# Kernel optimization log

Hardware: AMD Instinct MI355X
Metric: run time of the kernel (lower is better)

Reference implementation:

```python
import jax, jax.numpy as jnp
import numpy as np

NEG_SLOPE = 0.01  # F.leaky_relu default
DROP_P = 0.5      # F.dropout(p=0.5, training=True by default in this code)


def _lrelu(x):
    return jnp.where(x >= 0, x, NEG_SLOPE * x)


def _hconv(Xi, X, Ht, Hs, edge_w, theta, w_trans, bias):
    # Faithful to Ht.T @ diag(edge_w) @ Hs @ X @ theta + Xi @ w_trans + bias,
    # with diag(edge_w) fused as a per-row scale of the [E, out] intermediate.
    msg = (Hs @ X) @ theta                 # [E, out]
    agg = Ht.T @ (edge_w[:, None] * msg)   # [N, out]
    return _lrelu(agg + Xi @ w_trans + bias)


def setup_inputs() -> dict:
    key = jax.random.key(0)
    ks = jax.random.split(key, 14)
    N, E, F0, H = 8192, 4096, 128, 128
    f32 = jnp.float32
    return {
        "xi": jax.random.normal(ks[0], (N, F0), f32),
        "x": jax.random.normal(ks[1], (N, F0), f32),
        "Ht": jax.random.uniform(ks[2], (E, N), f32),
        "Hs": jax.random.uniform(ks[3], (E, N), f32),
        "state": jax.random.normal(ks[4], (N, 1), f32),
        # conv0 params (std=0.01 init as in torch code)
        "w_trans0": 0.01 * jax.random.normal(ks[5], (F0, H), f32),
        "theta0": 0.01 * jax.random.normal(ks[6], (F0, H), f32),
        "edge_w0": jnp.ones((E,), f32),
        "bias0": 0.01 * jax.random.normal(ks[7], (H,), f32),
        # conv1 params
        "w_trans1": 0.01 * jax.random.normal(ks[8], (H, H), f32),
        "theta1": 0.01 * jax.random.normal(ks[9], (H, H), f32),
        "edge_w1": jnp.ones((E,), f32),
        "bias1": 0.01 * jax.random.normal(ks[10], (H,), f32),
        # fc: Linear(H+1, 1)
        "fc_w": 0.01 * jax.random.normal(ks[11], (H + 1, 1), f32),
        "fc_b": 0.01 * jax.random.normal(ks[12], (1,), f32),
    }


def reference(xi, x, Ht, Hs, state,
              w_trans0, theta0, edge_w0, bias0,
              w_trans1, theta1, edge_w1, bias1,
              fc_w, fc_b):
    X1 = _hconv(xi, x, Ht, Hs, edge_w0, theta0, w_trans0, bias0)  # [N, H]
    # F.dropout(p=0.5) is active (training=True default); fixed mask for determinism
    keep = jax.random.bernoulli(jax.random.key(42), 1.0 - DROP_P, X1.shape)
    X1 = jnp.where(keep, X1 / (1.0 - DROP_P), 0.0)
    X2 = _hconv(xi, X1, Ht, Hs, edge_w1, theta1, w_trans1, bias1)  # [N, H]
    X = _lrelu(X2)  # second leaky_relu, as in DQN.forward
    Xc = jnp.concatenate([X, state], axis=1)  # [N, H+1]
    return Xc @ fc_w + fc_b  # [N, 1]
```

## Files before the change

### kernel.cpp

```cpp
#include <hip/hip_runtime.h>
#include <hip/hip_bf16.h>
#include <stdint.h>


typedef short short8 __attribute__((ext_vector_type(8)));
typedef float f32x4 __attribute__((ext_vector_type(4)));

static constexpr int N = 8192, E = 4096, F = 128;
static constexpr int SA = 8, SB = 4;

__device__ __forceinline__ unsigned rotl32(unsigned x, int r) {
  return (x << r) | (x >> (32 - r));
}

__device__ __forceinline__ uint2 threefry2x32(unsigned k0, unsigned k1,
                                              unsigned x0, unsigned x1) {
  unsigned ks[3] = {k0, k1, k0 ^ k1 ^ 0x1BD11BDAu};
  x0 += ks[0];
  x1 += ks[1];
  const int R0[4] = {13, 15, 26, 6};
  const int R1[4] = {17, 29, 16, 24};
#pragma unroll
  for (int i = 0; i < 5; ++i) {
#pragma unroll
    for (int j = 0; j < 4; ++j) {
      const int r = (i % 2 == 0) ? R0[j] : R1[j];
      x0 += x1;
      x1 = rotl32(x1, r);
      x1 ^= x0;
    }
    x0 += ks[(i + 1) % 3];
    x1 += ks[(i + 2) % 3] + (unsigned)(i + 1);
  }
  return make_uint2(x0, x1);
}

__device__ __forceinline__ float drop_scale(unsigned idx) {
  const uint2 o = threefry2x32(0u, 42u, 0u, idx);
  return ((o.x ^ o.y) & 0x80000000u) ? 0.0f : 2.0f;
}

__device__ __forceinline__ float lrelu(float v) {
  return v >= 0.0f ? v : 0.01f * v;
}

__device__ __forceinline__ unsigned rne1(float a) {
  unsigned ua = __builtin_bit_cast(unsigned, a);
  ua += 0x7fffu + ((ua >> 16) & 1u);
  return ua >> 16;
}
__device__ __forceinline__ float bf16_val(unsigned u16) {
  return __builtin_bit_cast(float, u16 << 16);
}
__device__ __forceinline__ unsigned pk_bf16(float a, float b) {
  return rne1(a) | (rne1(b) << 16);
}
__device__ __forceinline__ void split2(float a, float b, unsigned& hi,
                                       unsigned& lo) {
  const unsigned ha = rne1(a), hb = rne1(b);
  const float ra = a - bf16_val(ha), rb = b - bf16_val(hb);
  hi = ha | (hb << 16);
  lo = rne1(ra) | (rne1(rb) << 16);
}

template <bool TRANSA>
__global__ __launch_bounds__(256) void big_gemm(
    const float* __restrict__ A, const float* __restrict__ Bt,
    float* __restrict__ P, int M, int K, int lda, int kchunk) {
  __shared__ __align__(16) short As[128 * 40];
  __shared__ __align__(16) short Bh[128 * 40];
  __shared__ __align__(16) short Bl[128 * 40];

  const int tid = threadIdx.x;
  const int lane = tid & 63;
  const int w = tid >> 6;
  const int wm = (w & 1) << 6;
  const int wn = (w >> 1) << 6;
  const int l15 = lane & 15;
  const int koff = (lane >> 4) << 3;

  const int r0 = blockIdx.x * 128;
  const int s = blockIdx.y;
  const int kbeg = s * kchunk;
  const int kend = kbeg + kchunk;

  f32x4 acc[4][4];
#pragma unroll
  for (int i = 0; i < 4; ++i)
#pragma unroll
    for (int j = 0; j < 4; ++j) acc[i][j] = (f32x4){0.f, 0.f, 0.f, 0.f};

  for (int k0 = kbeg; k0 < kend; k0 += 32) {
    if (!TRANSA) {
#pragma unroll
      for (int i = 0; i < 4; ++i) {
        const int f = i * 256 + tid;
        const int m = f >> 3;
        const int kq = f & 7;
        const float4 v =
            *(const float4*)(A + (size_t)(r0 + m) * lda + k0 + 4 * kq);
        uint2 u = {pk_bf16(v.x, v.y), pk_bf16(v.z, v.w)};
        *(uint2*)&As[m * 40 + 4 * kq] = u;
      }
    } else {
#pragma unroll
      for (int i = 0; i < 2; ++i) {
        const int f = i * 256 + tid;
        const int m = f & 127;
        const int eo = f >> 7;
        float vv[8];
#pragma unroll
        for (int r = 0; r < 8; ++r)
          vv[r] = A[(size_t)(k0 + 8 * eo + r) * lda + (r0 + m)];
        uint4 u = {pk_bf16(vv[0], vv[1]), pk_bf16(vv[2], vv[3]),
                   pk_bf16(vv[4], vv[5]), pk_bf16(vv[6], vv[7])};
        *(uint4*)&As[m * 40 + 8 * eo] = u;
      }
    }
#pragma unroll
    for (int i = 0; i < 4; ++i) {
      const int q = i * 256 + tid;
      const int c = q >> 3;
      const int kq = q & 7;
      const float4 v = *(const float4*)(Bt + (size_t)c * K + k0 + 4 * kq);
      uint2 uh, ul;
      split2(v.x, v.y, uh.x, ul.x);
      split2(v.z, v.w, uh.y, ul.y);
      *(uint2*)&Bh[c * 40 + 4 * kq] = uh;
      *(uint2*)&Bl[c * 40 + 4 * kq] = ul;
    }
    __syncthreads();

    short8 af[4], bh[4], bl[4];
#pragma unroll
    for (int i = 0; i < 4; ++i)
      af[i] = *(const short8*)&As[(wm + 16 * i + l15) * 40 + koff];
#pragma unroll
    for (int j = 0; j < 4; ++j) {
      bh[j] = *(const short8*)&Bh[(wn + 16 * j + l15) * 40 + koff];
      bl[j] = *(const short8*)&Bl[(wn + 16 * j + l15) * 40 + koff];
    }
#pragma unroll
    for (int i = 0; i < 4; ++i)
#pragma unroll
      for (int j = 0; j < 4; ++j) {
        acc[i][j] = __builtin_amdgcn_mfma_f32_16x16x32_bf16(af[i], bl[j],
                                                            acc[i][j], 0, 0, 0);
        acc[i][j] = __builtin_amdgcn_mfma_f32_16x16x32_bf16(af[i], bh[j],
                                                            acc[i][j], 0, 0, 0);
      }
    __syncthreads();
  }

  const int rquad = (lane >> 4) << 2;
#pragma unroll
  for (int i = 0; i < 4; ++i)
#pragma unroll
    for (int j = 0; j < 4; ++j)
#pragma unroll
      for (int r = 0; r < 4; ++r) {
        const int row = r0 + wm + 16 * i + rquad + r;
        const int col = wn + 16 * j + l15;
        P[((size_t)s * M + row) * 128 + col] = acc[i][j][r];
      }
}

template <bool WA>
__global__ __launch_bounds__(256) void small_gemm(
    const float* __restrict__ src, const float* __restrict__ W,
    float* __restrict__ out) {
  __shared__ __align__(16) short WTh[128 * 40], WTl[128 * 40];
  __shared__ __align__(16) short Xh[64 * 40], Xl[64 * 40];

  const int tid = threadIdx.x;
  const int lane = tid & 63;
  const int w = tid >> 6;
  const int l15 = lane & 15;
  const int n0 = blockIdx.x * 64;

  constexpr int TI = WA ? 4 : 2;
  constexpr int TJ = WA ? 2 : 4;
  const int wm = (w & 1) * (WA ? 64 : 32);
  const int wn = (w >> 1) * (WA ? 32 : 64);

  f32x4 acc[TI][TJ];
#pragma unroll
  for (int i = 0; i < TI; ++i)
#pragma unroll
    for (int j = 0; j < TJ; ++j) acc[i][j] = (f32x4){0.f, 0.f, 0.f, 0.f};

  for (int k0 = 0; k0 < 128; k0 += 32) {
#pragma unroll
    for (int i = 0; i < 2; ++i) {
      const int f = i * 256 + tid;
      const int c = f & 127;
      const int eo = f >> 7;
      uint4 uh, ul;
      unsigned* ph = (unsigned*)&uh;
      unsigned* pl = (unsigned*)&ul;
#pragma unroll
      for (int r = 0; r < 4; ++r) {
        const float a = W[(size_t)(k0 + 8 * eo + 2 * r) * 128 + c];
        const float b = W[(size_t)(k0 + 8 * eo + 2 * r + 1) * 128 + c];
        split2(a, b, ph[r], pl[r]);
      }
      *(uint4*)&WTh[c * 40 + 8 * eo] = uh;
      *(uint4*)&WTl[c * 40 + 8 * eo] = ul;
    }
#pragma unroll
    for (int i = 0; i < 2; ++i) {
      const int q = i * 256 + tid;
      const int n = q >> 3;
      const int kq = q & 7;
      const float4 v = *(const float4*)(src + (size_t)(n0 + n) * 128 + k0 + 4 * kq);
      uint2 uh, ul;
      split2(v.x, v.y, uh.x, ul.x);
      split2(v.z, v.w, uh.y, ul.y);
      *(uint2*)&Xh[n * 40 + 4 * kq] = uh;
      *(uint2*)&Xl[n * 40 + 4 * kq] = ul;
    }
    __syncthreads();

    const int koff = (lane >> 4) << 3;
    short8 ah[TI], al[TI], bh[TJ], bl[TJ];
#pragma unroll
    for (int i = 0; i < TI; ++i) {
      const int m = wm + 16 * i + l15;
      ah[i] = WA ? *(const short8*)&WTh[m * 40 + koff]
                 : *(const short8*)&Xh[m * 40 + koff];
      al[i] = WA ? *(const short8*)&WTl[m * 40 + koff]
                 : *(const short8*)&Xl[m * 40 + koff];
    }
#pragma unroll
    for (int j = 0; j < TJ; ++j) {
      const int c = wn + 16 * j + l15;
      bh[j] = WA ? *(const short8*)&Xh[c * 40 + koff]
                 : *(const short8*)&WTh[c * 40 + koff];
      bl[j] = WA ? *(const short8*)&Xl[c * 40 + koff]
                 : *(const short8*)&WTl[c * 40 + koff];
    }
#pragma unroll
    for (int i = 0; i < TI; ++i)
#pragma unroll
      for (int j = 0; j < TJ; ++j) {
        acc[i][j] = __builtin_amdgcn_mfma_f32_16x16x32_bf16(al[i], bh[j],
                                                            acc[i][j], 0, 0, 0);
        acc[i][j] = __builtin_amdgcn_mfma_f32_16x16x32_bf16(ah[i], bl[j],
                                                            acc[i][j], 0, 0, 0);
        acc[i][j] = __builtin_amdgcn_mfma_f32_16x16x32_bf16(ah[i], bh[j],
                                                            acc[i][j], 0, 0, 0);
      }
    __syncthreads();
  }

  const int rquad = (lane >> 4) << 2;
#pragma unroll
  for (int i = 0; i < TI; ++i)
#pragma unroll
    for (int j = 0; j < TJ; ++j)
#pragma unroll
      for (int r = 0; r < 4; ++r) {
        const int row = wm + 16 * i + rquad + r;
        const int col = wn + 16 * j + l15;
        if (WA)
          out[(size_t)row * N + n0 + col] = acc[i][j][r];
        else
          out[(size_t)(n0 + row) * 128 + col] = acc[i][j][r];
      }
}

__global__ __launch_bounds__(256) void reduce_A(const float* __restrict__ P,
                                                const float* __restrict__ ew,
                                                float* __restrict__ Mt) {
  __shared__ float Lt[32 * 132];
  const int tid = threadIdx.x;
  const int e0 = blockIdx.x * 32;
#pragma unroll
  for (int i = 0; i < 4; ++i) {
    const int f = i * 256 + tid;
    const int el = f >> 5;
    const int cq = f & 31;
    float4 a = {0.f, 0.f, 0.f, 0.f};
#pragma unroll
    for (int s = 0; s < SA; ++s) {
      const float4 v =
          *(const float4*)(P + ((size_t)s * E + e0 + el) * 128 + 4 * cq);
      a.x += v.x; a.y += v.y; a.z += v.z; a.w += v.w;
    }
    const float sc = ew[e0 + el];
    a.x *= sc; a.y *= sc; a.z *= sc; a.w *= sc;
    *(float4*)&Lt[el * 132 + 4 * cq] = a;
  }
  __syncthreads();
#pragma unroll
  for (int i = 0; i < 4; ++i) {
    const int g = i * 256 + tid;
    const int c = g >> 3;
    const int eq = g & 7;
    float4 o;
    o.x = Lt[(4 * eq + 0) * 132 + c];
    o.y = Lt[(4 * eq + 1) * 132 + c];
    o.z = Lt[(4 * eq + 2) * 132 + c];
    o.w = Lt[(4 * eq + 3) * 132 + c];
    *(float4*)&Mt[(size_t)c * E + e0 + 4 * eq] = o;
  }
}

__global__ __launch_bounds__(256) void reduce_B1(const float* __restrict__ P,
                                                 const float* __restrict__ Badd,
                                                 const float* __restrict__ bias,
                                                 float* __restrict__ X1) {
  const int q = blockIdx.x * 256 + threadIdx.x;
  const int n = q >> 5;
  const int cq = q & 31;
  float4 a = {0.f, 0.f, 0.f, 0.f};
#pragma unroll
  for (int s = 0; s < SB; ++s) {
    const float4 v = *(const float4*)(P + ((size_t)s * N + n) * 128 + 4 * cq);
    a.x += v.x; a.y += v.y; a.z += v.z; a.w += v.w;
  }
  const float4 b = *(const float4*)(Badd + (size_t)n * 128 + 4 * cq);
  const float4 bi = *(const float4*)(bias + 4 * cq);
  const unsigned fb = (unsigned)(n * 128 + 4 * cq);
  float4 o;
  o.x = lrelu(a.x + b.x + bi.x) * drop_scale(fb + 0u);
  o.y = lrelu(a.y + b.y + bi.y) * drop_scale(fb + 1u);
  o.z = lrelu(a.z + b.z + bi.z) * drop_scale(fb + 2u);
  o.w = lrelu(a.w + b.w + bi.w) * drop_scale(fb + 3u);
  *(float4*)&X1[(size_t)n * 128 + 4 * cq] = o;
}

__global__ __launch_bounds__(256) void reduce_B2(
    const float* __restrict__ P, const float* __restrict__ Badd,
    const float* __restrict__ bias, const float* __restrict__ fcw,
    const float* __restrict__ state, const float* __restrict__ fcb,
    float* __restrict__ out) {
  __shared__ float part[4];
  const int tid = threadIdx.x;
  const int nn = tid >> 7;
  const int c = tid & 127;
  const int n = blockIdx.x * 2 + nn;
  float v = 0.f;
#pragma unroll
  for (int s = 0; s < SB; ++s) v += P[((size_t)s * N + n) * 128 + c];
  v += Badd[(size_t)n * 128 + c] + bias[c];
  float p = lrelu(lrelu(v)) * fcw[c];
#pragma unroll
  for (int m = 32; m >= 1; m >>= 1) p += __shfl_xor(p, m, 64);
  if ((tid & 63) == 0) part[tid >> 6] = p;
  __syncthreads();
  if (tid < 2)
    out[blockIdx.x * 2 + tid] = part[2 * tid] + part[2 * tid + 1] +
                                state[blockIdx.x * 2 + tid] * fcw[128] + fcb[0];
}

extern "C" void kernel_launch(void* const* d_in, const int* in_sizes, int n_in,
                              void* d_out, int out_size, void* d_ws,
                              size_t ws_size, hipStream_t stream) {
  (void)in_sizes; (void)n_in; (void)out_size; (void)ws_size;

  const float* xi = (const float*)d_in[0];
  const float* x = (const float*)d_in[1];
  const float* Ht = (const float*)d_in[2];
  const float* Hs = (const float*)d_in[3];
  const float* state = (const float*)d_in[4];
  const float* wt0 = (const float*)d_in[5];
  const float* th0 = (const float*)d_in[6];
  const float* ew0 = (const float*)d_in[7];
  const float* bi0 = (const float*)d_in[8];
  const float* wt1 = (const float*)d_in[9];
  const float* th1 = (const float*)d_in[10];
  const float* ew1 = (const float*)d_in[11];
  const float* bi1 = (const float*)d_in[12];
  const float* fcw = (const float*)d_in[13];
  const float* fcb = (const float*)d_in[14];
  float* out = (float*)d_out;

  float* ws = (float*)d_ws;
  float* P = ws;
  float* Tt = P + (size_t)4194304;
  float* Badd = Tt + (size_t)N * F;
  float* Mt = Badd + (size_t)N * F;
  float* X1 = Mt + (size_t)E * F;

  const dim3 blk(256);

  small_gemm<true><<<N / 64, blk, 0, stream>>>(x, th0, Tt);
  small_gemm<false><<<N / 64, blk, 0, stream>>>(xi, wt0, Badd);
  big_gemm<false><<<dim3(E / 128, SA), blk, 0, stream>>>(Hs, Tt, P, E, N, N,
                                                         N / SA);
  reduce_A<<<E / 32, blk, 0, stream>>>(P, ew0, Mt);
  big_gemm<true><<<dim3(N / 128, SB), blk, 0, stream>>>(Ht, Mt, P, N, E, N,
                                                        E / SB);
  reduce_B1<<<N * F / 4 / 256, blk, 0, stream>>>(P, Badd, bi0, X1);

  small_gemm<true><<<N / 64, blk, 0, stream>>>(X1, th1, Tt);
  small_gemm<false><<<N / 64, blk, 0, stream>>>(xi, wt1, Badd);
  big_gemm<false><<<dim3(E / 128, SA), blk, 0, stream>>>(Hs, Tt, P, E, N, N,
                                                         N / SA);
  reduce_A<<<E / 32, blk, 0, stream>>>(P, ew1, Mt);
  big_gemm<true><<<dim3(N / 128, SB), blk, 0, stream>>>(Ht, Mt, P, N, E, N,
                                                        E / SB);
  reduce_B2<<<N / 2, blk, 0, stream>>>(P, Badd, bi1, fcw, state, fcb, out);
}
```

Measured before the change: 521.7 us.

## Pre-split B operands to bf16 hi/lo, prefetch tiles, raise split-K when workspace allows

Small GEMM and reduce_A now write the B operands of the big GEMMs directly as bf16 hi/lo pairs, so big_gemm no longer converts fp32 to split bf16 on every tile and reads half the bytes per element. big_gemm register-prefetches the next A/B tiles while computing the current one, overlapping global loads with MFMA. Split-K factors double when the workspace is large enough, giving more blocks for occupancy at the cost of larger partial buffers and more reduction traffic.

```diff
diff --git a/kernel.cpp b/kernel.cpp
--- a/kernel.cpp
+++ b/kernel.cpp
@@ -6,8 +6,7 @@
 typedef short short8 __attribute__((ext_vector_type(8)));
 typedef float f32x4 __attribute__((ext_vector_type(4)));
 
-static constexpr int N = 8192, E = 4096, F = 128;
-static constexpr int SA = 8, SB = 4;
+static constexpr int N = 8192, E = 4096;
 
 __device__ __forceinline__ unsigned rotl32(unsigned x, int r) {
   return (x << r) | (x >> (32 - r));
@@ -62,14 +61,20 @@
   hi = ha | (hb << 16);
   lo = rne1(ra) | (rne1(rb) << 16);
 }
+__device__ __forceinline__ void split1(float a, unsigned& hi, unsigned& lo) {
+  const unsigned ha = rne1(a);
+  hi = ha;
+  lo = rne1(a - bf16_val(ha));
+}
 
 template <bool TRANSA>
 __global__ __launch_bounds__(256) void big_gemm(
-    const float* __restrict__ A, const float* __restrict__ Bt,
-    float* __restrict__ P, int M, int K, int lda, int kchunk) {
+    const float* __restrict__ A, const short* __restrict__ Bth,
+    const short* __restrict__ Btl, float* __restrict__ P, int M, int K,
+    int lda, int kchunk) {
   __shared__ __align__(16) short As[128 * 40];
-  __shared__ __align__(16) short Bh[128 * 40];
-  __shared__ __align__(16) short Bl[128 * 40];
+  __shared__ __align__(16) short Bhs[128 * 40];
+  __shared__ __align__(16) short Bls[128 * 40];
 
   const int tid = threadIdx.x;
   const int lane = tid & 63;
@@ -90,17 +95,18 @@
 #pragma unroll
     for (int j = 0; j < 4; ++j) acc[i][j] = (f32x4){0.f, 0.f, 0.f, 0.f};
 
-  for (int k0 = kbeg; k0 < kend; k0 += 32) {
+  float4 pa[4];
+  float pav[2][8];
+  uint4 pbh[2], pbl[2];
+
+  auto loadA = [&](int k0) {
     if (!TRANSA) {
 #pragma unroll
       for (int i = 0; i < 4; ++i) {
         const int f = i * 256 + tid;
         const int m = f >> 3;
         const int kq = f & 7;
-        const float4 v =
-            *(const float4*)(A + (size_t)(r0 + m) * lda + k0 + 4 * kq);
-        uint2 u = {pk_bf16(v.x, v.y), pk_bf16(v.z, v.w)};
-        *(uint2*)&As[m * 40 + 4 * kq] = u;
+        pa[i] = *(const float4*)(A + (size_t)(r0 + m) * lda + k0 + 4 * kq);
       }
     } else {
 #pragma unroll
@@ -108,37 +114,71 @@
         const int f = i * 256 + tid;
         const int m = f & 127;
         const int eo = f >> 7;
-        float vv[8];
 #pragma unroll
         for (int r = 0; r < 8; ++r)
-          vv[r] = A[(size_t)(k0 + 8 * eo + r) * lda + (r0 + m)];
-        uint4 u = {pk_bf16(vv[0], vv[1]), pk_bf16(vv[2], vv[3]),
-                   pk_bf16(vv[4], vv[5]), pk_bf16(vv[6], vv[7])};
+          pav[i][r] = A[(size_t)(k0 + 8 * eo + r) * lda + (r0 + m)];
+      }
+    }
+  };
+  auto loadB = [&](int k0) {
+#pragma unroll
+    for (int i = 0; i < 2; ++i) {
+      const int q = i * 256 + tid;
+      const int c = q >> 2;
+      const int kqo = q & 3;
+      pbh[i] = *(const uint4*)(Bth + (size_t)c * K + k0 + 8 * kqo);
+      pbl[i] = *(const uint4*)(Btl + (size_t)c * K + k0 + 8 * kqo);
+    }
+  };
+  auto storeLDS = [&]() {
+    if (!TRANSA) {
+#pragma unroll
+      for (int i = 0; i < 4; ++i) {
+        const int f = i * 256 + tid;
+        const int m = f >> 3;
+        const int kq = f & 7;
+        uint2 u = {pk_bf16(pa[i].x, pa[i].y), pk_bf16(pa[i].z, pa[i].w)};
+        *(uint2*)&As[m * 40 + 4 * kq] = u;
+      }
+    } else {
+#pragma unroll
+      for (int i = 0; i < 2; ++i) {
+        const int f = i * 256 + tid;
+        const int m = f & 127;
+        const int eo = f >> 7;
+        uint4 u = {pk_bf16(pav[i][0], pav[i][1]), pk_bf16(pav[i][2], pav[i][3]),
+                   pk_bf16(pav[i][4], pav[i][5]),
+                   pk_bf16(pav[i][6], pav[i][7])};
         *(uint4*)&As[m * 40 + 8 * eo] = u;
       }
     }
 #pragma unroll
-    for (int i = 0; i < 4; ++i) {
+    for (int i = 0; i < 2; ++i) {
       const int q = i * 256 + tid;
-      const int c = q >> 3;
-      const int kq = q & 7;
-      const float4 v = *(const float4*)(Bt + (size_t)c * K + k0 + 4 * kq);
-      uint2 uh, ul;
-      split2(v.x, v.y, uh.x, ul.x);
-      split2(v.z, v.w, uh.y, ul.y);
-      *(uint2*)&Bh[c * 40 + 4 * kq] = uh;
-      *(uint2*)&Bl[c * 40 + 4 * kq] = ul;
-    }
+      const int c = q >> 2;
+      const int kqo = q & 3;
+      *(uint4*)&Bhs[c * 40 + 8 * kqo] = pbh[i];
+      *(uint4*)&Bls[c * 40 + 8 * kqo] = pbl[i];
+    }
+  };
+
+  loadA(kbeg);
+  loadB(kbeg);
+  for (int k0 = kbeg; k0 < kend; k0 += 32) {
+    storeLDS();
     __syncthreads();
-
+    if (k0 + 32 < kend) {
+      loadA(k0 + 32);
+      loadB(k0 + 32);
+    }
     short8 af[4], bh[4], bl[4];
 #pragma unroll
     for (int i = 0; i < 4; ++i)
       af[i] = *(const short8*)&As[(wm + 16 * i + l15) * 40 + koff];
 #pragma unroll
     for (int j = 0; j < 4; ++j) {
-      bh[j] = *(const short8*)&Bh[(wn + 16 * j + l15) * 40 + koff];
-      bl[j] = *(const short8*)&Bl[(wn + 16 * j + l15) * 40 + koff];
+      bh[j] = *(const short8*)&Bhs[(wn + 16 * j + l15) * 40 + koff];
+      bl[j] = *(const short8*)&Bls[(wn + 16 * j + l15) * 40 + koff];
     }
 #pragma unroll
     for (int i = 0; i < 4; ++i)
@@ -168,7 +208,8 @@
 template <bool WA>
 __global__ __launch_bounds__(256) void small_gemm(
     const float* __restrict__ src, const float* __restrict__ W,
-    float* __restrict__ out) {
+    short* __restrict__ outh, short* __restrict__ outl,
+    float* __restrict__ outf) {
   __shared__ __align__(16) short WTh[128 * 40], WTl[128 * 40];
   __shared__ __align__(16) short Xh[64 * 40], Xl[64 * 40];
 
@@ -212,7 +253,8 @@
       const int q = i * 256 + tid;
       const int n = q >> 3;
       const int kq = q & 7;
-      const float4 v = *(const float4*)(src + (size_t)(n0 + n) * 128 + k0 + 4 * kq);
+      const float4 v =
+          *(const float4*)(src + (size_t)(n0 + n) * 128 + k0 + 4 * kq);
       uint2 uh, ul;
       split2(v.x, v.y, uh.x, ul.x);
       split2(v.z, v.w, uh.y, ul.y);
@@ -262,16 +304,23 @@
       for (int r = 0; r < 4; ++r) {
         const int row = wm + 16 * i + rquad + r;
         const int col = wn + 16 * j + l15;
-        if (WA)
-          out[(size_t)row * N + n0 + col] = acc[i][j][r];
-        else
-          out[(size_t)(n0 + row) * 128 + col] = acc[i][j][r];
+        const float v = acc[i][j][r];
+        if (WA) {
+          unsigned hi, lo;
+          split1(v, hi, lo);
+          outh[(size_t)row * N + n0 + col] = (short)hi;
+          outl[(size_t)row * N + n0 + col] = (short)lo;
+        } else {
+          outf[(size_t)(n0 + row) * 128 + col] = v;
+        }
       }
 }
 
 __global__ __launch_bounds__(256) void reduce_A(const float* __restrict__ P,
                                                 const float* __restrict__ ew,
-                                                float* __restrict__ Mt) {
+                                                short* __restrict__ Mth,
+                                                short* __restrict__ Mtl,
+                                                int S) {
   __shared__ float Lt[32 * 132];
   const int tid = threadIdx.x;
   const int e0 = blockIdx.x * 32;
@@ -281,8 +330,7 @@
     const int el = f >> 5;
     const int cq = f & 31;
     float4 a = {0.f, 0.f, 0.f, 0.f};
-#pragma unroll
-    for (int s = 0; s < SA; ++s) {
+    for (int s = 0; s < S; ++s) {
       const float4 v =
           *(const float4*)(P + ((size_t)s * E + e0 + el) * 128 + 4 * cq);
       a.x += v.x; a.y += v.y; a.z += v.z; a.w += v.w;
@@ -297,25 +345,28 @@
     const int g = i * 256 + tid;
     const int c = g >> 3;
     const int eq = g & 7;
-    float4 o;
-    o.x = Lt[(4 * eq + 0) * 132 + c];
-    o.y = Lt[(4 * eq + 1) * 132 + c];
-    o.z = Lt[(4 * eq + 2) * 132 + c];
-    o.w = Lt[(4 * eq + 3) * 132 + c];
-    *(float4*)&Mt[(size_t)c * E + e0 + 4 * eq] = o;
+    float o0 = Lt[(4 * eq + 0) * 132 + c];
+    float o1 = Lt[(4 * eq + 1) * 132 + c];
+    float o2 = Lt[(4 * eq + 2) * 132 + c];
+    float o3 = Lt[(4 * eq + 3) * 132 + c];
+    uint2 uh, ul;
+    split2(o0, o1, uh.x, ul.x);
+    split2(o2, o3, uh.y, ul.y);
+    *(uint2*)&Mth[(size_t)c * E + e0 + 4 * eq] = uh;
+    *(uint2*)&Mtl[(size_t)c * E + e0 + 4 * eq] = ul;
   }
 }
 
 __global__ __launch_bounds__(256) void reduce_B1(const float* __restrict__ P,
                                                  const float* __restrict__ Badd,
                                                  const float* __restrict__ bias,
-                                                 float* __restrict__ X1) {
+                                                 float* __restrict__ X1,
+                                                 int S) {
   const int q = blockIdx.x * 256 + threadIdx.x;
   const int n = q >> 5;
   const int cq = q & 31;
   float4 a = {0.f, 0.f, 0.f, 0.f};
-#pragma unroll
-  for (int s = 0; s < SB; ++s) {
+  for (int s = 0; s < S; ++s) {
     const float4 v = *(const float4*)(P + ((size_t)s * N + n) * 128 + 4 * cq);
     a.x += v.x; a.y += v.y; a.z += v.z; a.w += v.w;
   }
@@ -334,15 +385,14 @@
     const float* __restrict__ P, const float* __restrict__ Badd,
     const float* __restrict__ bias, const float* __restrict__ fcw,
     const float* __restrict__ state, const float* __restrict__ fcb,
-    float* __restrict__ out) {
+    float* __restrict__ out, int S) {
   __shared__ float part[4];
   const int tid = threadIdx.x;
   const int nn = tid >> 7;
   const int c = tid & 127;
   const int n = blockIdx.x * 2 + nn;
   float v = 0.f;
-#pragma unroll
-  for (int s = 0; s < SB; ++s) v += P[((size_t)s * N + n) * 128 + c];
+  for (int s = 0; s < S; ++s) v += P[((size_t)s * N + n) * 128 + c];
   v += Badd[(size_t)n * 128 + c] + bias[c];
   float p = lrelu(lrelu(v)) * fcw[c];
 #pragma unroll
@@ -357,7 +407,7 @@
 extern "C" void kernel_launch(void* const* d_in, const int* in_sizes, int n_in,
                               void* d_out, int out_size, void* d_ws,
                               size_t ws_size, hipStream_t stream) {
-  (void)in_sizes; (void)n_in; (void)out_size; (void)ws_size;
+  (void)in_sizes; (void)n_in; (void)out_size;
 
   const float* xi = (const float*)d_in[0];
   const float* x = (const float*)d_in[1];
@@ -376,30 +426,40 @@
   const float* fcb = (const float*)d_in[14];
   float* out = (float*)d_out;
 
-  float* ws = (float*)d_ws;
-  float* P = ws;
-  float* Tt = P + (size_t)4194304;
-  float* Badd = Tt + (size_t)N * F;
-  float* Mt = Badd + (size_t)N * F;
-  float* X1 = Mt + (size_t)E * F;
+  const bool big_ws = ws_size >= ((size_t)48 << 20);
+  const int SAe = big_ws ? 16 : 8;
+  const int SBe = big_ws ? 8 : 4;
+  const size_t Pfloats = (size_t)SAe * E * 128;
+
+  char* wsb = (char*)d_ws;
+  float* P = (float*)wsb;
+  short* Tth = (short*)(wsb + Pfloats * 4);
+  short* Ttl = Tth + (size_t)128 * N;
+  short* Mth = Ttl + (size_t)128 * N;
+  short* Mtl = Mth + (size_t)128 * E;
+  float* Badd = (float*)(Mtl + (size_t)128 * E);
+  float* X1 = Badd + (size_t)N * 128;
 
   const dim3 blk(256);
 
-  small_gemm<true><<<N / 64, blk, 0, stream>>>(x, th0, Tt);
-  small_gemm<false><<<N / 64, blk, 0, stream>>>(xi, wt0, Badd);
-  big_gemm<false><<<dim3(E / 128, SA), blk, 0, stream>>>(Hs, Tt, P, E, N, N,
-                                                         N / SA);
-  reduce_A<<<E / 32, blk, 0, stream>>>(P, ew0, Mt);
-  big_gemm<true><<<dim3(N / 128, SB), blk, 0, stream>>>(Ht, Mt, P, N, E, N,
-                                                        E / SB);
-  reduce_B1<<<N * F / 4 / 256, blk, 0, stream>>>(P, Badd, bi0, X1);
-
-  small_gemm<true><<<N / 64, blk, 0, stream>>>(X1, th1, Tt);
-  small_gemm<false><<<N / 64, blk, 0, stream>>>(xi, wt1, Badd);
-  big_gemm<false><<<dim3(E / 128, SA), blk, 0, stream>>>(Hs, Tt, P, E, N, N,
-                                                         N / SA);
-  reduce_A<<<E / 32, blk, 0, stream>>>(P, ew1, Mt);
-  big_gemm<true><<<dim3(N / 128, SB), blk, 0, stream>>>(Ht, Mt, P, N, E, N,
-                                                        E / SB);
-  reduce_B2<<<N / 2, blk, 0, stream>>>(P, Badd, bi1, fcw, state, fcb, out);
-}
+  small_gemm<true><<<N / 64, blk, 0, stream>>>(x, th0, Tth, Ttl, nullptr);
+  small_gemm<false><<<N / 64, blk, 0, stream>>>(xi, wt0, nullptr, nullptr,
+                                                Badd);
+  big_gemm<false><<<dim3(E / 128, SAe), blk, 0, stream>>>(Hs, Tth, Ttl, P, E,
+                                                          N, N, N / SAe);
+  reduce_A<<<E / 32, blk, 0, stream>>>(P, ew0, Mth, Mtl, SAe);
+  big_gemm<true><<<dim3(N / 128, SBe), blk, 0, stream>>>(Ht, Mth, Mtl, P, N,
+                                                         E, N, E / SBe);
+  reduce_B1<<<N * 128 / 4 / 256, blk, 0, stream>>>(P, Badd, bi0, X1, SBe);
+
+  small_gemm<true><<<N / 64, blk, 0, stream>>>(X1, th1, Tth, Ttl, nullptr);
+  small_gemm<false><<<N / 64, blk, 0, stream>>>(xi, wt1, nullptr, nullptr,
+                                                Badd);
+  big_gemm<false><<<dim3(E / 128, SAe), blk, 0, stream>>>(Hs, Tth, Ttl, P, E,
+                                                          N, N, N / SAe);
+  reduce_A<<<E / 32, blk, 0, stream>>>(P, ew1, Mth, Mtl, SAe);
+  big_gemm<true><<<dim3(N / 128, SBe), blk, 0, stream>>>(Ht, Mth, Mtl, P, N,
+                                                         E, N, E / SBe);
+  reduce_B2<<<N / 2, blk, 0, stream>>>(P, Badd, bi1, fcw, state, fcb, out,
+                                       SBe);
+}
```

Result: slower. 608.1 us (+16.6%).
